# Kernel optimization log

Hardware: AMD Instinct MI355X
Metric: run time of the kernel (lower is better)

## Reference

```python
import jax, jax.numpy as jnp
import numpy as np

B, T, C, H = 2, 2048, 1024, 16
HD = C // H          # head_dim = 64
RD = HD // 2         # rotary half-dim = 32


def _rope_tables(T, rd, base=10000.0):
    inv_freq = 1.0 / (base ** (np.arange(rd, dtype=np.float32) / rd))
    t = np.arange(T, dtype=np.float32)
    ang = np.outer(t, inv_freq)  # [T, rd]
    cos = np.cos(ang)[None, :, None, :]  # [1,T,1,rd]
    sin = np.sin(ang)[None, :, None, :]
    return jnp.asarray(cos), jnp.asarray(sin)


def setup_inputs() -> dict:
    key = jax.random.key(0)
    k1, k2, k3 = jax.random.split(key, 3)
    cos, sin = _rope_tables(T, RD)
    return {
        "x": jax.random.normal(k1, (B, T, C), dtype=jnp.float32),
        "cos": cos,
        "sin": sin,
        "W_qkv": jax.random.normal(k2, (C, C), dtype=jnp.float32) / np.sqrt(C),
        "W_proj": jax.random.normal(k3, (C, C), dtype=jnp.float32) / np.sqrt(C),
        "window_left": 512,
    }


def _apply_rotary(x, cos, sin):
    # x: [B,T,H,HD]
    x1, x2 = x[..., :RD], x[..., RD:]
    y1 = x1 * cos + x2 * sin
    y2 = -x1 * sin + x2 * cos
    return jnp.concatenate([y1, y2], axis=-1)


def _rms_norm(x):
    eps = jnp.finfo(x.dtype).eps
    ms = jnp.mean(jnp.square(x), axis=-1, keepdims=True)
    return x * jax.lax.rsqrt(ms + eps)


def reference(x, cos, sin, W_qkv, W_proj, window_left):
    Bx, Tx, Cx = x.shape
    scale = HD ** -0.5
    # tied QKV projection (single matmul)
    w = jnp.einsum("btc,cd->btd", x, W_qkv).reshape(Bx, Tx, H, HD)
    w = _apply_rotary(w, cos, sin)
    w = _rms_norm(w)                      # [B,T,H,HD]
    wq = jnp.transpose(w, (0, 2, 1, 3))    # [B,H,T,HD]
    dots = jnp.einsum("bhqd,bhkd->bhqk", wq, wq) * scale  # [B,H,T,T]
    # causal + sliding-window mask: allow 0 <= (q - k) <= window_left
    i = jnp.arange(Tx)[:, None]
    j = jnp.arange(Tx)[None, :]
    dist = i - j
    allowed = (dist >= 0) & ((window_left <= 0) | (dist <= window_left))
    dots = jnp.where(allowed, dots, -jnp.inf)
    attn = jax.nn.softmax(dots, axis=-1)
    out = jnp.einsum("bhqk,bhkd->bhqd", attn, wq)
    out = jnp.transpose(out, (0, 2, 1, 3)).reshape(Bx, Tx, Cx)
    return jnp.einsum("btc,cd->btd", out, W_proj)
```

## Files before the change

### kernel.cpp

```cpp
#include <hip/hip_runtime.h>
#include <hip/hip_bf16.h>

typedef __bf16 bf16_t;
typedef __bf16 bf16x4 __attribute__((ext_vector_type(4)));
typedef __bf16 bf16x8 __attribute__((ext_vector_type(8)));
typedef float f32x4 __attribute__((ext_vector_type(4)));

#define B_ 2
#define T_ 2048
#define C_ 1024
#define H_ 16
#define HD_ 64
#define RD_ 32
#define M_ (B_ * T_)

__global__ __launch_bounds__(256) void k_prep(const float* __restrict__ x,
                                              bf16_t* __restrict__ xb,
                                              const float* __restrict__ Wq,
                                              bf16_t* __restrict__ wqt,
                                              const float* __restrict__ Wp,
                                              bf16_t* __restrict__ wpt) {
    const int bid = blockIdx.x;
    if (bid < 4096) {
        int i = bid * 256 + threadIdx.x;
        float4 v = reinterpret_cast<const float4*>(x)[i];
        bf16x4 o;
        o[0] = (bf16_t)v.x; o[1] = (bf16_t)v.y; o[2] = (bf16_t)v.z; o[3] = (bf16_t)v.w;
        reinterpret_cast<bf16x4*>(xb)[i] = o;
    } else {
        __shared__ float tile[32][33];
        int b2 = bid - 4096;
        const float* W = (b2 < 1024) ? Wq : Wp;
        bf16_t* Wt = (b2 < 1024) ? wqt : wpt;
        b2 &= 1023;
        const int n0 = (b2 & 31) * 32, k0 = (b2 >> 5) * 32;
        const int tx = threadIdx.x & 31, ty = threadIdx.x >> 5;
        for (int i = ty; i < 32; i += 8)
            tile[i][tx] = W[(size_t)(k0 + i) * C_ + n0 + tx];
        __syncthreads();
        for (int i = ty; i < 32; i += 8)
            Wt[(size_t)(n0 + i) * C_ + k0 + tx] = (bf16_t)tile[tx][i];
    }
}

template <bool FUSED>
__global__ __launch_bounds__(256) void k_gemm(const bf16_t* __restrict__ A,
                                              const bf16_t* __restrict__ Bt,
                                              float* __restrict__ C,
                                              const float* __restrict__ ct,
                                              const float* __restrict__ st,
                                              bf16_t* __restrict__ qp,
                                              bf16_t* __restrict__ vp,
                                              int M, int N, int K) {
    __shared__ __align__(16) char smem[73728];
    bf16_t* As = (bf16_t*)smem;
    bf16_t* Bs = (bf16_t*)(smem + 49152);
    const int tid = threadIdx.x;
    const int lane = tid & 63, w = tid >> 6;
    const int wr = w >> 1, wc = w & 1;
    const int g = lane >> 4, li = lane & 15;
    const int bid = blockIdx.x;
    int bx, by;
    if constexpr (FUSED) {
        const int xcd = bid & 7, i = bid >> 3;
        bx = (xcd & 3) * 4 + (i & 3);
        by = (xcd >> 2) * 16 + (i >> 2);
    } else {
        const int work = (bid & 7) * 64 + (bid >> 3);
        bx = work & 15;
        by = work >> 4;
    }
    const size_t rowA0 = (size_t)by * 128;
    const size_t colB0 = (size_t)bx * 64;
    const bf16_t* Ab = A + rowA0 * K;
    const bf16_t* Bb = Bt + colB0 * K;
    f32x4 acc[4][2] = {};

    const int lr = lane >> 3;
    const int swc = ((lane & 7) ^ lr) * 8;

    auto stage = [&](int buf, int k0) {
        bf16_t* Ad = As + buf * 8192 + (w * 8) * 64;
        bf16_t* Bd = Bs + buf * 4096 + (w * 8) * 64;
#pragma unroll
        for (int a = 0; a < 4; ++a) {
            const bf16_t* src = Ab + (size_t)(a * 32 + w * 8 + lr) * K + k0 + swc;
            __builtin_amdgcn_global_load_lds(
                (const __attribute__((address_space(1))) void*)src,
                (__attribute__((address_space(3))) void*)(Ad + a * 32 * 64), 16, 0, 0);
        }
#pragma unroll
        for (int bq = 0; bq < 2; ++bq) {
            const bf16_t* src = Bb + (size_t)(bq * 32 + w * 8 + lr) * K + k0 + swc;
            __builtin_amdgcn_global_load_lds(
                (const __attribute__((address_space(1))) void*)src,
                (__attribute__((address_space(3))) void*)(Bd + bq * 32 * 64), 16, 0, 0);
        }
    };

    const int NT = K >> 6;
    stage(0, 0);
    stage(1, 64);
    for (int kt = 0; kt < NT; ++kt) {
        if (kt + 1 < NT)
            asm volatile("s_waitcnt vmcnt(6)" ::: "memory");
        else
            asm volatile("s_waitcnt vmcnt(0)" ::: "memory");
        __builtin_amdgcn_s_barrier();
        if (kt + 2 < NT) stage((kt + 2) % 3, (kt + 2) << 6);
        const int cb = kt % 3;
        bf16x8 af[4][2], bfr[2][2];
#pragma unroll
        for (int i = 0; i < 4; ++i) {
            const int row = wr * 64 + i * 16 + li;
#pragma unroll
            for (int kk = 0; kk < 2; ++kk)
                af[i][kk] = *(const bf16x8*)(As + cb * 8192 + row * 64 +
                                             (((kk * 4 + g) ^ (li & 7)) * 8));
        }
#pragma unroll
        for (int j = 0; j < 2; ++j) {
            const int row = wc * 32 + j * 16 + li;
#pragma unroll
            for (int kk = 0; kk < 2; ++kk)
                bfr[j][kk] = *(const bf16x8*)(Bs + cb * 4096 + row * 64 +
                                              (((kk * 4 + g) ^ (li & 7)) * 8));
        }
#pragma unroll
        for (int i = 0; i < 4; ++i)
#pragma unroll
            for (int j = 0; j < 2; ++j)
#pragma unroll
                for (int kk = 0; kk < 2; ++kk)
                    acc[i][j] = __builtin_amdgcn_mfma_f32_16x16x32_bf16(
                        af[i][kk], bfr[j][kk], acc[i][j], 0, 0, 0);
    }

    if constexpr (!FUSED) {
#pragma unroll
        for (int i = 0; i < 4; ++i)
#pragma unroll
            for (int j = 0; j < 2; ++j)
#pragma unroll
                for (int r = 0; r < 4; ++r) {
                    size_t row = rowA0 + wr * 64 + i * 16 + g * 4 + r;
                    size_t col = colB0 + wc * 32 + j * 16 + li;
                    C[row * N + col] = acc[i][j][r];
                }
    } else {
        __syncthreads();
        float* ot = (float*)smem;
        bf16_t* qs = (bf16_t*)(smem + 34816);
#pragma unroll
        for (int i = 0; i < 4; ++i)
#pragma unroll
            for (int j = 0; j < 2; ++j)
#pragma unroll
                for (int r = 0; r < 4; ++r)
                    ot[(wr * 64 + i * 16 + g * 4 + r) * 68 + wc * 32 + j * 16 + li] =
                        acc[i][j][r];
        __syncthreads();
        const int bb = (int)(rowA0 >> 11);
        {
            const int row = tid >> 1, half = tid & 1;
            const int t = ((int)rowA0 + row) & 2047;
            const float* own = ot + row * 68 + half * 32;
            const float* par = ot + row * 68 + (half ^ 1) * 32;
            const float* cp = ct + (size_t)t * RD_;
            const float* sp = st + (size_t)t * RD_;
            float y[32];
            float sq = 0.f;
#pragma unroll
            for (int c4 = 0; c4 < 8; ++c4) {
                float4 xo = ((const float4*)own)[c4];
                float4 xp = ((const float4*)par)[c4];
                float4 cc = ((const float4*)cp)[c4];
                float4 ss = ((const float4*)sp)[c4];
                float* yy = y + c4 * 4;
                if (half == 0) {
                    yy[0] = xo.x * cc.x + xp.x * ss.x;
                    yy[1] = xo.y * cc.y + xp.y * ss.y;
                    yy[2] = xo.z * cc.z + xp.z * ss.z;
                    yy[3] = xo.w * cc.w + xp.w * ss.w;
                } else {
                    yy[0] = xo.x * cc.x - xp.x * ss.x;
                    yy[1] = xo.y * cc.y - xp.y * ss.y;
                    yy[2] = xo.z * cc.z - xp.z * ss.z;
                    yy[3] = xo.w * cc.w - xp.w * ss.w;
                }
                sq += yy[0] * yy[0] + yy[1] * yy[1] + yy[2] * yy[2] + yy[3] * yy[3];
            }
            sq += __shfl_xor(sq, 1);
            const float rn = rsqrtf(sq * (1.0f / 64.0f) + 1.1920929e-7f);
            bf16_t yb[32];
#pragma unroll
            for (int e = 0; e < 32; ++e) yb[e] = (bf16_t)(y[e] * rn);
            bf16_t* qpb = qp + ((size_t)(bb * H_ + bx) * 128 + (t >> 4)) * 1024;
#pragma unroll
            for (int c8 = 0; c8 < 4; ++c8) {
                const int chunk = (half * 4 + c8) * 16 + (t & 15);
                *(bf16x8*)(qpb + chunk * 8) = *(const bf16x8*)(yb + c8 * 8);
            }
#pragma unroll
            for (int e = 0; e < 32; ++e)
                qs[(half * 32 + e) * 136 + row] = yb[e];
        }
        __syncthreads();
        {
            const int d = tid >> 2, jc4 = tid & 3;
            const int tt0 = (int)((rowA0 & 2047) >> 6);
            bf16_t* vpb = vp + ((size_t)(bb * H_ + bx) * 32) * 4096;
#pragma unroll
            for (int c = 0; c < 4; ++c) {
                const int jc = jc4 * 4 + c;
                bf16x8 v8 = *(const bf16x8*)(qs + d * 136 + jc * 8);
                bf16_t* dst = vpb + (size_t)(tt0 + (jc >> 3)) * 4096 +
                              ((d >> 4) * 8 + (jc & 7)) * 128 + (d & 15) * 8;
                *(bf16x8*)dst = v8;
            }
        }
    }
}

__global__ __launch_bounds__(256, 2) void k_attn(const bf16_t* __restrict__ qp,
                                                 const bf16_t* __restrict__ vp,
                                                 bf16_t* __restrict__ aout,
                                                 const int* __restrict__ wlp) {
    __shared__ bf16_t pb[4][16][40];
    const int tid = threadIdx.x;
    const int lane = tid & 63, w = tid >> 6;
    const int g = lane >> 4, li = lane & 15;
    const int bid = blockIdx.x;
    const int work = (bid & 7) * 128 + (bid >> 3);
    const int tb = work & 31;
    const int h = (work >> 5) & 15;
    const int b = work >> 9;
    const int Q0 = tb * 64;
    const bf16_t* bq = qp + (size_t)(b * H_ + h) * 131072;
    const bf16_t* bv = vp + (size_t)(b * H_ + h) * 131072;
    const int wl = wlp[0];
    const int wle = (wl <= 0 || wl > T_) ? T_ : wl;
    const int qw = Q0 + w * 16;
    const int qg = qw + li;

    const int fo = (g * 16 + li) * 8;
    const int vo = g * 128 + li * 8;

    bf16x8 aq[2];
    aq[0] = *(const bf16x8*)(bq + (size_t)(qw >> 4) * 1024 + fo);
    aq[1] = *(const bf16x8*)(bq + (size_t)(qw >> 4) * 1024 + fo + 512);

    f32x4 o[4] = {};
    float m = -1e30f, l = 0.f;
    const float SC = 0.125f * 1.44269504089f;

    const int kb0 = (qw > wle) ? ((qw - wle) >> 6) : 0;
    const int kb1 = qw >> 6;

    for (int kb = kb0; kb <= kb1; ++kb) {
        const int J0 = kb << 6;
        const bf16_t* kt = bq + (size_t)kb * 4096;
        const bf16_t* vt = bv + (size_t)kb * 4096;
        bf16x8 kf[2][4];
#pragma unroll
        for (int ks = 0; ks < 2; ++ks)
#pragma unroll
            for (int nb = 0; nb < 4; ++nb)
                kf[ks][nb] = *(const bf16x8*)(kt + nb * 1024 + ks * 512 + fo);
        f32x4 s4[4] = {};
        __builtin_amdgcn_s_setprio(1);
#pragma unroll
        for (int ks = 0; ks < 2; ++ks)
#pragma unroll
            for (int nb = 0; nb < 4; ++nb)
                s4[nb] = __builtin_amdgcn_mfma_f32_16x16x32_bf16(kf[ks][nb], aq[ks],
                                                                 s4[nb], 0, 0, 0);
        __builtin_amdgcn_s_setprio(0);
        bf16x8 vf[2][4];
#pragma unroll
        for (int ks = 0; ks < 2; ++ks)
#pragma unroll
            for (int dnb = 0; dnb < 4; ++dnb)
                vf[ks][dnb] = *(const bf16x8*)(vt + dnb * 1024 + ks * 512 + vo);
        float mn = m;
#pragma unroll
        for (int nb = 0; nb < 4; ++nb)
#pragma unroll
            for (int r = 0; r < 4; ++r) {
                const int j = J0 + nb * 16 + g * 4 + r;
                const int dist = qg - j;
                float x = s4[nb][r] * SC;
                s4[nb][r] = (dist >= 0 && dist <= wle) ? x : -__builtin_inff();
                mn = fmaxf(mn, s4[nb][r]);
            }
        mn = fmaxf(mn, __shfl_xor(mn, 16));
        mn = fmaxf(mn, __shfl_xor(mn, 32));
        const float al = exp2f(m - mn);
        m = mn;
        float la = 0.f;
#pragma unroll
        for (int nb = 0; nb < 4; ++nb)
#pragma unroll
            for (int r = 0; r < 4; ++r) {
                float pv = exp2f(s4[nb][r] - m);
                s4[nb][r] = pv;
                la += pv;
            }
        la += __shfl_xor(la, 16);
        la += __shfl_xor(la, 32);
        l = l * al + la;
        float alq[4];
#pragma unroll
        for (int r = 0; r < 4; ++r) alq[r] = __shfl(al, g * 4 + r);
#pragma unroll
        for (int dnb = 0; dnb < 4; ++dnb)
#pragma unroll
            for (int r = 0; r < 4; ++r) o[dnb][r] *= alq[r];
#pragma unroll
        for (int ks = 0; ks < 2; ++ks) {
#pragma unroll
            for (int nb2 = 0; nb2 < 2; ++nb2) {
                const int nb = ks * 2 + nb2;
                bf16x4 pk;
                pk[0] = (bf16_t)s4[nb][0]; pk[1] = (bf16_t)s4[nb][1];
                pk[2] = (bf16_t)s4[nb][2]; pk[3] = (bf16_t)s4[nb][3];
                *reinterpret_cast<bf16x4*>(&pb[w][li][nb2 * 16 + g * 4]) = pk;
            }
            bf16x8 pa = *reinterpret_cast<const bf16x8*>(&pb[w][li][g * 8]);
            __builtin_amdgcn_s_setprio(1);
#pragma unroll
            for (int dnb = 0; dnb < 4; ++dnb)
                o[dnb] = __builtin_amdgcn_mfma_f32_16x16x32_bf16(pa, vf[ks][dnb],
                                                                 o[dnb], 0, 0, 0);
            __builtin_amdgcn_s_setprio(0);
        }
    }

    const float rli = 1.0f / l;
    float rlq[4];
#pragma unroll
    for (int r = 0; r < 4; ++r) rlq[r] = __shfl(rli, g * 4 + r);
#pragma unroll
    for (int dnb = 0; dnb < 4; ++dnb)
#pragma unroll
        for (int r = 0; r < 4; ++r) {
            size_t t = (size_t)qw + g * 4 + r;
            aout[((size_t)b * T_ + t) * C_ + h * 64 + dnb * 16 + li] =
                (bf16_t)(o[dnb][r] * rlq[r]);
        }
}

extern "C" void kernel_launch(void* const* d_in, const int* in_sizes, int n_in,
                              void* d_out, int out_size, void* d_ws, size_t ws_size,
                              hipStream_t stream) {
    const float* x     = (const float*)d_in[0];
    const float* ct    = (const float*)d_in[1];
    const float* st    = (const float*)d_in[2];
    const float* Wqkv  = (const float*)d_in[3];
    const float* Wproj = (const float*)d_in[4];
    const int*   wl    = (const int*)d_in[5];
    float* out = (float*)d_out;
    char* ws = (char*)d_ws;

    bf16_t* xb    = (bf16_t*)(ws);
    bf16_t* wqkvt = (bf16_t*)(ws + (8ull << 20));
    bf16_t* wprot = (bf16_t*)(ws + (10ull << 20));
    bf16_t* qp    = (bf16_t*)(ws + (12ull << 20));
    bf16_t* vp    = (bf16_t*)(ws + (20ull << 20));
    bf16_t* ao    = (bf16_t*)(ws + (28ull << 20));

    k_prep<<<dim3(6144), dim3(256), 0, stream>>>(x, xb, Wqkv, wqkvt, Wproj, wprot);
    k_gemm<true><<<dim3(512), dim3(256), 0, stream>>>(xb, wqkvt, nullptr, ct, st,
                                                      qp, vp, M_, C_, C_);
    k_attn<<<dim3(1024), dim3(256), 0, stream>>>(qp, vp, ao, wl);
    k_gemm<false><<<dim3(512), dim3(256), 0, stream>>>(ao, wprot, out, nullptr, nullptr,
                                                       nullptr, nullptr, M_, C_, C_);
}
```

Measured before the change: 67.50 us.

## Fuse fp32-to-bf16 conversion of x into the QKV GEMM A-tile loader

```diff
diff --git a/kernel.cpp b/kernel.cpp
--- a/kernel.cpp
+++ b/kernel.cpp
@@ -14,62 +14,220 @@
 #define RD_ 32
 #define M_ (B_ * T_)
 
-__global__ __launch_bounds__(256) void k_prep(const float* __restrict__ x,
-                                              bf16_t* __restrict__ xb,
-                                              const float* __restrict__ Wq,
+__global__ __launch_bounds__(256) void k_prep(const float* __restrict__ Wq,
                                               bf16_t* __restrict__ wqt,
                                               const float* __restrict__ Wp,
                                               bf16_t* __restrict__ wpt) {
-    const int bid = blockIdx.x;
-    if (bid < 4096) {
-        int i = bid * 256 + threadIdx.x;
-        float4 v = reinterpret_cast<const float4*>(x)[i];
-        bf16x4 o;
-        o[0] = (bf16_t)v.x; o[1] = (bf16_t)v.y; o[2] = (bf16_t)v.z; o[3] = (bf16_t)v.w;
-        reinterpret_cast<bf16x4*>(xb)[i] = o;
-    } else {
-        __shared__ float tile[32][33];
-        int b2 = bid - 4096;
-        const float* W = (b2 < 1024) ? Wq : Wp;
-        bf16_t* Wt = (b2 < 1024) ? wqt : wpt;
-        b2 &= 1023;
-        const int n0 = (b2 & 31) * 32, k0 = (b2 >> 5) * 32;
-        const int tx = threadIdx.x & 31, ty = threadIdx.x >> 5;
-        for (int i = ty; i < 32; i += 8)
-            tile[i][tx] = W[(size_t)(k0 + i) * C_ + n0 + tx];
-        __syncthreads();
-        for (int i = ty; i < 32; i += 8)
-            Wt[(size_t)(n0 + i) * C_ + k0 + tx] = (bf16_t)tile[tx][i];
-    }
+    __shared__ float tile[32][33];
+    int b2 = blockIdx.x;
+    const float* W = (b2 < 1024) ? Wq : Wp;
+    bf16_t* Wt = (b2 < 1024) ? wqt : wpt;
+    b2 &= 1023;
+    const int n0 = (b2 & 31) * 32, k0 = (b2 >> 5) * 32;
+    const int tx = threadIdx.x & 31, ty = threadIdx.x >> 5;
+    for (int i = ty; i < 32; i += 8)
+        tile[i][tx] = W[(size_t)(k0 + i) * C_ + n0 + tx];
+    __syncthreads();
+    for (int i = ty; i < 32; i += 8)
+        Wt[(size_t)(n0 + i) * C_ + k0 + tx] = (bf16_t)tile[tx][i];
 }
 
-template <bool FUSED>
-__global__ __launch_bounds__(256) void k_gemm(const bf16_t* __restrict__ A,
-                                              const bf16_t* __restrict__ Bt,
-                                              float* __restrict__ C,
-                                              const float* __restrict__ ct,
-                                              const float* __restrict__ st,
-                                              bf16_t* __restrict__ qp,
-                                              bf16_t* __restrict__ vp,
-                                              int M, int N, int K) {
-    __shared__ __align__(16) char smem[73728];
+__global__ __launch_bounds__(256) void k_gemm1(const float* __restrict__ x,
+                                               const bf16_t* __restrict__ Bt,
+                                               const float* __restrict__ ct,
+                                               const float* __restrict__ st,
+                                               bf16_t* __restrict__ qp,
+                                               bf16_t* __restrict__ vp) {
+    __shared__ __align__(16) char smem[57344];
     bf16_t* As = (bf16_t*)smem;
-    bf16_t* Bs = (bf16_t*)(smem + 49152);
+    bf16_t* Bs = (bf16_t*)(smem + 32768);
+    const int K = C_;
     const int tid = threadIdx.x;
     const int lane = tid & 63, w = tid >> 6;
     const int wr = w >> 1, wc = w & 1;
     const int g = lane >> 4, li = lane & 15;
     const int bid = blockIdx.x;
-    int bx, by;
-    if constexpr (FUSED) {
-        const int xcd = bid & 7, i = bid >> 3;
-        bx = (xcd & 3) * 4 + (i & 3);
-        by = (xcd >> 2) * 16 + (i >> 2);
-    } else {
-        const int work = (bid & 7) * 64 + (bid >> 3);
-        bx = work & 15;
-        by = work >> 4;
+    const int xcd = bid & 7, i0 = bid >> 3;
+    const int bx = (xcd & 3) * 4 + (i0 & 3);
+    const int by = (xcd >> 2) * 16 + (i0 >> 2);
+    const size_t rowA0 = (size_t)by * 128;
+    const size_t colB0 = (size_t)bx * 64;
+    const float* Ab = x + rowA0 * K;
+    const bf16_t* Bb = Bt + colB0 * K;
+    f32x4 acc[4][2] = {};
+
+    const int lr = lane >> 3;
+    const int swc = ((lane & 7) ^ lr) * 8;
+
+    const int arow = tid >> 1, ahalf = tid & 1;
+
+    auto stageB = [&](int buf, int k0) {
+        bf16_t* Bd = Bs + buf * 4096 + (w * 8) * 64;
+#pragma unroll
+        for (int bq = 0; bq < 2; ++bq) {
+            const bf16_t* src = Bb + (size_t)(bq * 32 + w * 8 + lr) * K + k0 + swc;
+            __builtin_amdgcn_global_load_lds(
+                (const __attribute__((address_space(1))) void*)src,
+                (__attribute__((address_space(3))) void*)(Bd + bq * 32 * 64), 16, 0, 0);
+        }
+    };
+    auto loadA = [&](int k0, f32x4* ar) {
+        const float* src = Ab + (size_t)arow * K + k0 + ahalf * 32;
+#pragma unroll
+        for (int c = 0; c < 8; ++c) ar[c] = ((const f32x4*)src)[c];
+    };
+    auto writeA = [&](int buf, const f32x4* ar) {
+        bf16_t* base = As + buf * 8192 + arow * 64;
+#pragma unroll
+        for (int c = 0; c < 4; ++c) {
+            bf16x8 ch;
+#pragma unroll
+            for (int e = 0; e < 4; ++e) {
+                ch[e]     = (bf16_t)ar[c * 2][e];
+                ch[e + 4] = (bf16_t)ar[c * 2 + 1][e];
+            }
+            const int gc = ahalf * 4 + c;
+            *(bf16x8*)(base + ((gc ^ (arow & 7)) * 8)) = ch;
+        }
+    };
+
+    const int NT = K >> 6;
+    f32x4 ar[8];
+    loadA(0, ar);
+    stageB(0, 0);
+    stageB(1, 64);
+    asm volatile("s_waitcnt vmcnt(2)" ::: "memory");
+    writeA(0, ar);
+    asm volatile("s_waitcnt lgkmcnt(0)" ::: "memory");
+    __builtin_amdgcn_s_barrier();
+
+    for (int kt = 0; kt < NT; ++kt) {
+        if (kt + 1 < NT) loadA((kt + 1) << 6, ar);
+        if (kt + 2 < NT) stageB((kt + 2) % 3, (kt + 2) << 6);
+        const int ca = kt & 1, cb = kt % 3;
+        bf16x8 af[4][2], bfr[2][2];
+#pragma unroll
+        for (int i = 0; i < 4; ++i) {
+            const int row = wr * 64 + i * 16 + li;
+#pragma unroll
+            for (int kk = 0; kk < 2; ++kk)
+                af[i][kk] = *(const bf16x8*)(As + ca * 8192 + row * 64 +
+                                             (((kk * 4 + g) ^ (row & 7)) * 8));
+        }
+#pragma unroll
+        for (int j = 0; j < 2; ++j) {
+            const int row = wc * 32 + j * 16 + li;
+#pragma unroll
+            for (int kk = 0; kk < 2; ++kk)
+                bfr[j][kk] = *(const bf16x8*)(Bs + cb * 4096 + row * 64 +
+                                              (((kk * 4 + g) ^ (row & 7)) * 8));
+        }
+#pragma unroll
+        for (int i = 0; i < 4; ++i)
+#pragma unroll
+            for (int j = 0; j < 2; ++j)
+#pragma unroll
+                for (int kk = 0; kk < 2; ++kk)
+                    acc[i][j] = __builtin_amdgcn_mfma_f32_16x16x32_bf16(
+                        af[i][kk], bfr[j][kk], acc[i][j], 0, 0, 0);
+        if (kt + 1 < NT) {
+            if (kt + 2 < NT)
+                asm volatile("s_waitcnt vmcnt(2)" ::: "memory");
+            else
+                asm volatile("s_waitcnt vmcnt(0)" ::: "memory");
+            writeA((kt + 1) & 1, ar);
+        }
+        asm volatile("s_waitcnt lgkmcnt(0)" ::: "memory");
+        __builtin_amdgcn_s_barrier();
     }
+
+    float* ot = (float*)smem;
+    bf16_t* qs = (bf16_t*)(smem + 34816);
+#pragma unroll
+    for (int i = 0; i < 4; ++i)
+#pragma unroll
+        for (int j = 0; j < 2; ++j)
+#pragma unroll
+            for (int r = 0; r < 4; ++r)
+                ot[(wr * 64 + i * 16 + g * 4 + r) * 68 + wc * 32 + j * 16 + li] =
+                    acc[i][j][r];
+    __syncthreads();
+    const int bb = (int)(rowA0 >> 11);
+    {
+        const int row = tid >> 1, half = tid & 1;
+        const int t = ((int)rowA0 + row) & 2047;
+        const float* own = ot + row * 68 + half * 32;
+        const float* par = ot + row * 68 + (half ^ 1) * 32;
+        const float* cp = ct + (size_t)t * RD_;
+        const float* sp = st + (size_t)t * RD_;
+        float y[32];
+        float sq = 0.f;
+#pragma unroll
+        for (int c4 = 0; c4 < 8; ++c4) {
+            float4 xo = ((const float4*)own)[c4];
+            float4 xp = ((const float4*)par)[c4];
+            float4 cc = ((const float4*)cp)[c4];
+            float4 ss = ((const float4*)sp)[c4];
+            float* yy = y + c4 * 4;
+            if (half == 0) {
+                yy[0] = xo.x * cc.x + xp.x * ss.x;
+                yy[1] = xo.y * cc.y + xp.y * ss.y;
+                yy[2] = xo.z * cc.z + xp.z * ss.z;
+                yy[3] = xo.w * cc.w + xp.w * ss.w;
+            } else {
+                yy[0] = xo.x * cc.x - xp.x * ss.x;
+                yy[1] = xo.y * cc.y - xp.y * ss.y;
+                yy[2] = xo.z * cc.z - xp.z * ss.z;
+                yy[3] = xo.w * cc.w - xp.w * ss.w;
+            }
+            sq += yy[0] * yy[0] + yy[1] * yy[1] + yy[2] * yy[2] + yy[3] * yy[3];
+        }
+        sq += __shfl_xor(sq, 1);
+        const float rn = rsqrtf(sq * (1.0f / 64.0f) + 1.1920929e-7f);
+        bf16_t yb[32];
+#pragma unroll
+        for (int e = 0; e < 32; ++e) yb[e] = (bf16_t)(y[e] * rn);
+        bf16_t* qpb = qp + ((size_t)(bb * H_ + bx) * 128 + (t >> 4)) * 1024;
+#pragma unroll
+        for (int c8 = 0; c8 < 4; ++c8) {
+            const int chunk = (half * 4 + c8) * 16 + (t & 15);
+            *(bf16x8*)(qpb + chunk * 8) = *(const bf16x8*)(yb + c8 * 8);
+        }
+#pragma unroll
+        for (int e = 0; e < 32; ++e)
+            qs[(half * 32 + e) * 136 + row] = yb[e];
+    }
+    __syncthreads();
+    {
+        const int d = tid >> 2, jc4 = tid & 3;
+        const int tt0 = (int)((rowA0 & 2047) >> 6);
+        bf16_t* vpb = vp + ((size_t)(bb * H_ + bx) * 32) * 4096;
+#pragma unroll
+        for (int c = 0; c < 4; ++c) {
+            const int jc = jc4 * 4 + c;
+            bf16x8 v8 = *(const bf16x8*)(qs + d * 136 + jc * 8);
+            bf16_t* dst = vpb + (size_t)(tt0 + (jc >> 3)) * 4096 +
+                          ((d >> 4) * 8 + (jc & 7)) * 128 + (d & 15) * 8;
+            *(bf16x8*)dst = v8;
+        }
+    }
+}
+
+__global__ __launch_bounds__(256) void k_gemm2(const bf16_t* __restrict__ A,
+                                               const bf16_t* __restrict__ Bt,
+                                               float* __restrict__ C) {
+    __shared__ __align__(16) char smem[73728];
+    bf16_t* As = (bf16_t*)smem;
+    bf16_t* Bs = (bf16_t*)(smem + 49152);
+    const int K = C_, N = C_;
+    const int tid = threadIdx.x;
+    const int lane = tid & 63, w = tid >> 6;
+    const int wr = w >> 1, wc = w & 1;
+    const int g = lane >> 4, li = lane & 15;
+    const int bid = blockIdx.x;
+    const int work = (bid & 7) * 64 + (bid >> 3);
+    const int bx = work & 15;
+    const int by = work >> 4;
     const size_t rowA0 = (size_t)by * 128;
     const size_t colB0 = (size_t)bx * 64;
     const bf16_t* Ab = A + rowA0 * K;
@@ -116,7 +274,7 @@
 #pragma unroll
             for (int kk = 0; kk < 2; ++kk)
                 af[i][kk] = *(const bf16x8*)(As + cb * 8192 + row * 64 +
-                                             (((kk * 4 + g) ^ (li & 7)) * 8));
+                                             (((kk * 4 + g) ^ (row & 7)) * 8));
         }
 #pragma unroll
         for (int j = 0; j < 2; ++j) {
@@ -124,7 +282,7 @@
 #pragma unroll
             for (int kk = 0; kk < 2; ++kk)
                 bfr[j][kk] = *(const bf16x8*)(Bs + cb * 4096 + row * 64 +
-                                              (((kk * 4 + g) ^ (li & 7)) * 8));
+                                              (((kk * 4 + g) ^ (row & 7)) * 8));
         }
 #pragma unroll
         for (int i = 0; i < 4; ++i)
@@ -135,91 +293,16 @@
                     acc[i][j] = __builtin_amdgcn_mfma_f32_16x16x32_bf16(
                         af[i][kk], bfr[j][kk], acc[i][j], 0, 0, 0);
     }
-
-    if constexpr (!FUSED) {
-#pragma unroll
-        for (int i = 0; i < 4; ++i)
-#pragma unroll
-            for (int j = 0; j < 2; ++j)
-#pragma unroll
-                for (int r = 0; r < 4; ++r) {
-                    size_t row = rowA0 + wr * 64 + i * 16 + g * 4 + r;
-                    size_t col = colB0 + wc * 32 + j * 16 + li;
-                    C[row * N + col] = acc[i][j][r];
-                }
-    } else {
-        __syncthreads();
-        float* ot = (float*)smem;
-        bf16_t* qs = (bf16_t*)(smem + 34816);
-#pragma unroll
-        for (int i = 0; i < 4; ++i)
-#pragma unroll
-            for (int j = 0; j < 2; ++j)
-#pragma unroll
-                for (int r = 0; r < 4; ++r)
-                    ot[(wr * 64 + i * 16 + g * 4 + r) * 68 + wc * 32 + j * 16 + li] =
-                        acc[i][j][r];
-        __syncthreads();
-        const int bb = (int)(rowA0 >> 11);
-        {
-            const int row = tid >> 1, half = tid & 1;
-            const int t = ((int)rowA0 + row) & 2047;
-            const float* own = ot + row * 68 + half * 32;
-            const float* par = ot + row * 68 + (half ^ 1) * 32;
-            const float* cp = ct + (size_t)t * RD_;
-            const float* sp = st + (size_t)t * RD_;
-            float y[32];
-            float sq = 0.f;
-#pragma unroll
-            for (int c4 = 0; c4 < 8; ++c4) {
-                float4 xo = ((const float4*)own)[c4];
-                float4 xp = ((const float4*)par)[c4];
-                float4 cc = ((const float4*)cp)[c4];
-                float4 ss = ((const float4*)sp)[c4];
-                float* yy = y + c4 * 4;
-                if (half == 0) {
-                    yy[0] = xo.x * cc.x + xp.x * ss.x;
-                    yy[1] = xo.y * cc.y + xp.y * ss.y;
-                    yy[2] = xo.z * cc.z + xp.z * ss.z;
-                    yy[3] = xo.w * cc.w + xp.w * ss.w;
-                } else {
-                    yy[0] = xo.x * cc.x - xp.x * ss.x;
-                    yy[1] = xo.y * cc.y - xp.y * ss.y;
-                    yy[2] = xo.z * cc.z - xp.z * ss.z;
-                    yy[3] = xo.w * cc.w - xp.w * ss.w;
-                }
-                sq += yy[0] * yy[0] + yy[1] * yy[1] + yy[2] * yy[2] + yy[3] * yy[3];
-            }
-            sq += __shfl_xor(sq, 1);
-            const float rn = rsqrtf(sq * (1.0f / 64.0f) + 1.1920929e-7f);
-            bf16_t yb[32];
-#pragma unroll
-            for (int e = 0; e < 32; ++e) yb[e] = (bf16_t)(y[e] * rn);
-            bf16_t* qpb = qp + ((size_t)(bb * H_ + bx) * 128 + (t >> 4)) * 1024;
-#pragma unroll
-            for (int c8 = 0; c8 < 4; ++c8) {
-                const int chunk = (half * 4 + c8) * 16 + (t & 15);
-                *(bf16x8*)(qpb + chunk * 8) = *(const bf16x8*)(yb + c8 * 8);
-            }
-#pragma unroll
-            for (int e = 0; e < 32; ++e)
-                qs[(half * 32 + e) * 136 + row] = yb[e];
-        }
-        __syncthreads();
-        {
-            const int d = tid >> 2, jc4 = tid & 3;
-            const int tt0 = (int)((rowA0 & 2047) >> 6);
-            bf16_t* vpb = vp + ((size_t)(bb * H_ + bx) * 32) * 4096;
-#pragma unroll
-            for (int c = 0; c < 4; ++c) {
-                const int jc = jc4 * 4 + c;
-                bf16x8 v8 = *(const bf16x8*)(qs + d * 136 + jc * 8);
-                bf16_t* dst = vpb + (size_t)(tt0 + (jc >> 3)) * 4096 +
-                              ((d >> 4) * 8 + (jc & 7)) * 128 + (d & 15) * 8;
-                *(bf16x8*)dst = v8;
-            }
-        }
-    }
+#pragma unroll
+    for (int i = 0; i < 4; ++i)
+#pragma unroll
+        for (int j = 0; j < 2; ++j)
+#pragma unroll
+            for (int r = 0; r < 4; ++r) {
+                size_t row = rowA0 + wr * 64 + i * 16 + g * 4 + r;
+                size_t col = colB0 + wc * 32 + j * 16 + li;
+                C[row * N + col] = acc[i][j][r];
+            }
 }
 
 __global__ __launch_bounds__(256, 2) void k_attn(const bf16_t* __restrict__ qp,
@@ -289,8 +372,8 @@
             for (int r = 0; r < 4; ++r) {
                 const int j = J0 + nb * 16 + g * 4 + r;
                 const int dist = qg - j;
-                float x = s4[nb][r] * SC;
-                s4[nb][r] = (dist >= 0 && dist <= wle) ? x : -__builtin_inff();
+                float xv = s4[nb][r] * SC;
+                s4[nb][r] = (dist >= 0 && dist <= wle) ? xv : -__builtin_inff();
                 mn = fmaxf(mn, s4[nb][r]);
             }
         mn = fmaxf(mn, __shfl_xor(mn, 16));
@@ -362,17 +445,14 @@
     float* out = (float*)d_out;
     char* ws = (char*)d_ws;
 
-    bf16_t* xb    = (bf16_t*)(ws);
     bf16_t* wqkvt = (bf16_t*)(ws + (8ull << 20));
     bf16_t* wprot = (bf16_t*)(ws + (10ull << 20));
     bf16_t* qp    = (bf16_t*)(ws + (12ull << 20));
     bf16_t* vp    = (bf16_t*)(ws + (20ull << 20));
     bf16_t* ao    = (bf16_t*)(ws + (28ull << 20));
 
-    k_prep<<<dim3(6144), dim3(256), 0, stream>>>(x, xb, Wqkv, wqkvt, Wproj, wprot);
-    k_gemm<true><<<dim3(512), dim3(256), 0, stream>>>(xb, wqkvt, nullptr, ct, st,
-                                                      qp, vp, M_, C_, C_);
+    k_prep<<<dim3(2048), dim3(256), 0, stream>>>(Wqkv, wqkvt, Wproj, wprot);
+    k_gemm1<<<dim3(512), dim3(256), 0, stream>>>(x, wqkvt, ct, st, qp, vp);
     k_attn<<<dim3(1024), dim3(256), 0, stream>>>(qp, vp, ao, wl);
-    k_gemm<false><<<dim3(512), dim3(256), 0, stream>>>(ao, wprot, out, nullptr, nullptr,
-                                                       nullptr, nullptr, M_, C_, C_);
+    k_gemm2<<<dim3(512), dim3(256), 0, stream>>>(ao, wprot, out);
 }
```

After: 94.75 us. 1.4x slower.
